# Optimization experiments

Measured on AMD Instinct MI355X. Metric: run time of the kernel, lower is better.

## Reference

```python
import jax, jax.numpy as jnp
import numpy as np

GROUP_SIZE = 64

def setup_inputs() -> dict:
    key = jax.random.key(0)
    ks = jax.random.split(key, 7)
    T, N, K, NG = 4096, 4096, 11264, 4096 // GROUP_SIZE
    x = jax.random.normal(ks[0], (T, N), dtype=jnp.float32)
    Q = jax.random.randint(ks[1], (K, N), 0, 8, dtype=jnp.int32)  # uint8 3-bit codes
    scales = jax.random.uniform(ks[2], (K, NG), dtype=jnp.float32)
    zeros = jax.random.uniform(ks[3], (K, NG), dtype=jnp.float32) * 7.0
    mu1 = jax.random.uniform(ks[4], (N,), dtype=jnp.float32) + 0.5
    mu2 = jax.random.uniform(ks[5], (K,), dtype=jnp.float32) + 0.5
    bias = jax.random.normal(ks[6], (K,), dtype=jnp.float32)
    return {"x": x, "Q": Q, "scales": scales, "zeros": zeros, "mu1": mu1, "mu2": mu2, "bias": bias}

def reference(x, Q, scales, zeros, mu1, mu2, bias):
    K, N = Q.shape
    ng = scales.shape[1]
    # group-wise dequant: (Q - zero) * scale, groups along N
    Qg = Q.astype(jnp.float32).reshape(K, ng, GROUP_SIZE)
    W_deq_norm = ((Qg - zeros[:, :, None]) * scales[:, :, None]).reshape(K, N)
    # Sinkhorn mu rescale: per-row mu2, per-column mu1
    W_deq = W_deq_norm * mu2[:, None] * mu1[None, :]
    out = x @ W_deq.T + bias
    return out
```

## Files before the change

kernel.cpp:

```cpp
#include <hip/hip_runtime.h>
#include <stdint.h>
#include <stddef.h>


typedef __attribute__((ext_vector_type(8))) short bfrag;
typedef __attribute__((ext_vector_type(4))) short s16x4;
typedef __attribute__((ext_vector_type(4))) float f32x4;
typedef __attribute__((ext_vector_type(4))) int   i32x4;

__device__ __forceinline__ short f2bf(float f) {
    uint32_t u = __float_as_uint(f);
    u += 0x7fffu + ((u >> 16) & 1u);
    return (short)(u >> 16);
}

__device__ __forceinline__ void gload_lds16(const void* g, void* l) {
    __builtin_amdgcn_global_load_lds(
        (const __attribute__((address_space(1))) void*)g,
        (__attribute__((address_space(3))) void*)l,
        16, 0, 0);
}

__global__ void cvt_x_kernel(const float* __restrict__ x, short* __restrict__ xb,
                             int total4) {
    for (int i = blockIdx.x * 256 + threadIdx.x; i < total4;
         i += gridDim.x * 256) {
        f32x4 a = ((const f32x4*)x)[i];
        s16x4 o;
        o[0] = f2bf(a[0]); o[1] = f2bf(a[1]);
        o[2] = f2bf(a[2]); o[3] = f2bf(a[3]);
        ((s16x4*)xb)[i] = o;
    }
}

__global__ void deq_w_kernel(const int* __restrict__ Q,
                             const float* __restrict__ scales,
                             const float* __restrict__ zeros,
                             const float* __restrict__ mu1,
                             const float* __restrict__ mu2,
                             short* __restrict__ wb,
                             int k0, int N, int NG) {
    const int kl = blockIdx.x;
    const int kg = k0 + kl;
    const float m2 = mu2[kg];
    const int*   qrow = Q + (size_t)kg * N;
    const float* srow = scales + (size_t)kg * NG;
    const float* zrow = zeros + (size_t)kg * NG;
    short*       orow = wb + (size_t)kl * N;
    for (int n0 = threadIdx.x * 4; n0 < N; n0 += 1024) {
        const int g = n0 >> 6;
        const float s = srow[g] * m2;
        const float z = zrow[g];
        i32x4 q = *(const i32x4*)(qrow + n0);
        f32x4 u = *(const f32x4*)(mu1 + n0);
        s16x4 o;
        o[0] = f2bf(((float)q[0] - z) * s * u[0]);
        o[1] = f2bf(((float)q[1] - z) * s * u[1]);
        o[2] = f2bf(((float)q[2] - z) * s * u[2]);
        o[3] = f2bf(((float)q[3] - z) * s * u[3]);
        *(s16x4*)(orow + n0) = o;
    }
}


__global__ __launch_bounds__(512, 2)
void gemm8p_kernel(const short* __restrict__ A, const short* __restrict__ B,
                   const float* __restrict__ bias, float* __restrict__ C,
                   int Kc, int Nout, int col0, int GX) {
    extern __shared__ __attribute__((aligned(16))) char smem[];

    const int tid  = threadIdx.x;
    const int lane = tid & 63;
    const int wid  = tid >> 6;
    const int wm   = wid >> 2;
    const int wn   = wid & 3;
    const int r    = lane & 15;
    const int hib  = (lane >> 4) << 4;
    const int sw   = (r & 7) << 4;

    const int nwg = (int)gridDim.x;
    const int cpx = nwg >> 3;
    const int bid = (int)blockIdx.x;
    const int swz = (bid & 7) * cpx + (bid >> 3);
    const int bx  = swz % GX;
    const int by  = swz / GX;
    const int bm  = by * 256;
    const int bnl = bx * 256;

    const int KB = Kc * 2;
    const int swcol = ((tid ^ (tid >> 3)) & 7) << 4;
    const char* srcA = (const char*)A + (size_t)(bm  + (tid >> 3)) * KB + swcol;
    const char* srcB = (const char*)B + (size_t)(bnl + (tid >> 3)) * KB + swcol;

    f32x4 acc[8][4];
#pragma unroll
    for (int i = 0; i < 8; i++)
#pragma unroll
        for (int j = 0; j < 4; j++)
            acc[i][j] = (f32x4){0.f, 0.f, 0.f, 0.f};

    const int NT = Kc / 64;

#define STG_A(t, q) gload_lds16(srcA + (size_t)(t) * 128 + (size_t)(q) * 64 * KB, \
                                smem + ((t) & 1) * 65536 + (q) * 8192 + (tid << 4))
#define STG_B(t, q) gload_lds16(srcB + (size_t)(t) * 128 + (size_t)(q) * 64 * KB, \
                                smem + ((t) & 1) * 65536 + 32768 + (q) * 8192 + (tid << 4))
#define LDF(base, row, s) (*(const bfrag*)((base) + (size_t)(row) * 128 + (((s) * 64 + hib) ^ sw)))
#define MM(I, J, AF, BF) acc[I][J] = __builtin_amdgcn_mfma_f32_16x16x32_bf16(AF, BF, acc[I][J], 0, 0, 0)

#define RD_A(Ab_, MQ) do { const int ra_ = wm * 128 + (MQ) * 64 + r;            \
    Af[0] = LDF(Ab_, ra_,      0); Af[1] = LDF(Ab_, ra_,      1);               \
    Af[2] = LDF(Ab_, ra_ + 16, 0); Af[3] = LDF(Ab_, ra_ + 16, 1);               \
    Af[4] = LDF(Ab_, ra_ + 32, 0); Af[5] = LDF(Ab_, ra_ + 32, 1);               \
    Af[6] = LDF(Ab_, ra_ + 48, 0); Af[7] = LDF(Ab_, ra_ + 48, 1); } while (0)

#define RD_B(Bb_, NQ, BF) do { const int rb_ = wn * 64 + (NQ) * 32 + r;         \
    BF[0] = LDF(Bb_, rb_,      0); BF[1] = LDF(Bb_, rb_,      1);               \
    BF[2] = LDF(Bb_, rb_ + 16, 0); BF[3] = LDF(Bb_, rb_ + 16, 1); } while (0)

#define QUAD(MQ, NQ, BF) do {                                                   \
    __builtin_amdgcn_s_barrier();                                               \
    asm volatile("s_waitcnt lgkmcnt(0)" ::: "memory");                          \
    __builtin_amdgcn_s_setprio(1);                                              \
    MM((MQ)*4 + 0, (NQ)*2 + 0, Af[0], BF[0]); MM((MQ)*4 + 0, (NQ)*2 + 0, Af[1], BF[1]); \
    MM((MQ)*4 + 0, (NQ)*2 + 1, Af[0], BF[2]); MM((MQ)*4 + 0, (NQ)*2 + 1, Af[1], BF[3]); \
    MM((MQ)*4 + 1, (NQ)*2 + 0, Af[2], BF[0]); MM((MQ)*4 + 1, (NQ)*2 + 0, Af[3], BF[1]); \
    MM((MQ)*4 + 1, (NQ)*2 + 1, Af[2], BF[2]); MM((MQ)*4 + 1, (NQ)*2 + 1, Af[3], BF[3]); \
    MM((MQ)*4 + 2, (NQ)*2 + 0, Af[4], BF[0]); MM((MQ)*4 + 2, (NQ)*2 + 0, Af[5], BF[1]); \
    MM((MQ)*4 + 2, (NQ)*2 + 1, Af[4], BF[2]); MM((MQ)*4 + 2, (NQ)*2 + 1, Af[5], BF[3]); \
    MM((MQ)*4 + 3, (NQ)*2 + 0, Af[6], BF[0]); MM((MQ)*4 + 3, (NQ)*2 + 0, Af[7], BF[1]); \
    MM((MQ)*4 + 3, (NQ)*2 + 1, Af[6], BF[2]); MM((MQ)*4 + 3, (NQ)*2 + 1, Af[7], BF[3]); \
    __builtin_amdgcn_s_setprio(0);                                              \
} while (0)

    STG_A(0, 0); STG_A(0, 1); STG_A(0, 2); STG_A(0, 3);
    STG_B(0, 0); STG_B(0, 1); STG_B(0, 2); STG_B(0, 3);
    STG_A(1, 0); STG_A(1, 2);
    asm volatile("s_waitcnt vmcnt(2)" ::: "memory");
    __builtin_amdgcn_s_barrier();

    bfrag Af[8], B0f[4], B1f[4];

    for (int it = 0; it < NT / 2; ++it) {
        const int tb = 2 * it + 1;
        int tc = 2 * it + 2; if (tc > NT - 1) tc = NT - 1;
        int td = 2 * it + 3; if (td > NT - 1) td = NT - 1;
        const char* Ab0 = smem;
        const char* Bb0 = smem + 32768;
        const char* Ab1 = smem + 65536;
        const char* Bb1 = smem + 98304;

        RD_A(Ab0, 0); RD_B(Bb0, 0, B0f);
        STG_A(tb, 1); STG_A(tb, 3); STG_B(tb, 0);
        QUAD(0, 0, B0f);
        __builtin_amdgcn_s_barrier();

        RD_B(Bb0, 1, B1f);
        STG_B(tb, 1); STG_B(tb, 2); STG_B(tb, 3);
        QUAD(0, 1, B1f);
        __builtin_amdgcn_s_barrier();

        RD_A(Ab0, 1);
        STG_A(tc, 0); STG_A(tc, 2);
        QUAD(1, 1, B1f);
        __builtin_amdgcn_s_barrier();

        QUAD(1, 0, B0f);
        asm volatile("s_waitcnt vmcnt(2)" ::: "memory");
        __builtin_amdgcn_s_barrier();

        RD_A(Ab1, 0); RD_B(Bb1, 0, B0f);
        STG_A(tc, 1); STG_A(tc, 3); STG_B(tc, 0);
        QUAD(0, 0, B0f);
        __builtin_amdgcn_s_barrier();

        RD_B(Bb1, 1, B1f);
        STG_B(tc, 1); STG_B(tc, 2); STG_B(tc, 3);
        QUAD(0, 1, B1f);
        __builtin_amdgcn_s_barrier();

        RD_A(Ab1, 1);
        STG_A(td, 0); STG_A(td, 2);
        QUAD(1, 1, B1f);
        __builtin_amdgcn_s_barrier();

        QUAD(1, 0, B0f);
        asm volatile("s_waitcnt vmcnt(2)" ::: "memory");
        __builtin_amdgcn_s_barrier();
    }

#undef QUAD
#undef RD_B
#undef RD_A
#undef MM
#undef LDF
#undef STG_B
#undef STG_A

    const int row0 = bm + wm * 128 + (lane >> 4) * 4;
    const int colg = col0 + bnl + wn * 64 + r;
#pragma unroll
    for (int j = 0; j < 4; ++j) {
        const int col = colg + j * 16;
        const float bv = bias[col];
#pragma unroll
        for (int i = 0; i < 8; ++i) {
            const int row = row0 + i * 16;
#pragma unroll
            for (int q = 0; q < 4; ++q)
                C[(size_t)(row + q) * Nout + col] = acc[i][j][q] + bv;
        }
    }
}

__global__ void naive_kernel(const float* __restrict__ x, const int* __restrict__ Q,
                             const float* __restrict__ scales, const float* __restrict__ zeros,
                             const float* __restrict__ mu1, const float* __restrict__ mu2,
                             const float* __restrict__ bias, float* __restrict__ out,
                             int T, int N, int K, int NG) {
    long long total = (long long)T * K;
    for (long long idx = blockIdx.x * 256ll + threadIdx.x; idx < total;
         idx += (long long)gridDim.x * 256ll) {
        int t = (int)(idx / K);
        int k = (int)(idx - (long long)t * K);
        float s = 0.f;
        for (int n = 0; n < N; n++) {
            int g = n >> 6;
            float w = ((float)Q[(size_t)k * N + n] - zeros[(size_t)k * NG + g]) *
                      scales[(size_t)k * NG + g];
            s += x[(size_t)t * N + n] * w * mu1[n];
        }
        out[idx] = s * mu2[k] + bias[k];
    }
}

extern "C" void kernel_launch(void* const* d_in, const int* in_sizes, int n_in,
                              void* d_out, int out_size, void* d_ws, size_t ws_size,
                              hipStream_t stream) {
    const float* x      = (const float*)d_in[0];
    const int*   Q      = (const int*)d_in[1];
    const float* scales = (const float*)d_in[2];
    const float* zeros  = (const float*)d_in[3];
    const float* mu1    = (const float*)d_in[4];
    const float* mu2    = (const float*)d_in[5];
    const float* bias   = (const float*)d_in[6];
    float* out = (float*)d_out;

    const int N  = in_sizes[4];
    const int K  = in_sizes[5];
    const int T  = in_sizes[0] / N;
    const int NG = in_sizes[2] / K;

    const size_t xb_bytes  = (size_t)T * N * 2;
    const size_t row_bytes = (size_t)N * 2;

    const bool shape_ok = (T % 256 == 0) && (K % 256 == 0) &&
                          (N % 1024 == 0) && (N % 128 == 0);

    if (!shape_ok || ws_size < xb_bytes + 256 * row_bytes) {
        naive_kernel<<<4096, 256, 0, stream>>>(x, Q, scales, zeros, mu1, mu2,
                                               bias, out, T, N, K, NG);
        return;
    }

    static bool attr_done = false;
    if (!attr_done) {
        (void)hipFuncSetAttribute(reinterpret_cast<const void*>(gemm8p_kernel),
                                  hipFuncAttributeMaxDynamicSharedMemorySize,
                                  131072);
        attr_done = true;
    }

    short* xb = (short*)d_ws;
    short* wb = (short*)((char*)d_ws + xb_bytes);
    size_t max_rows = (ws_size - xb_bytes) / row_bytes;
    int CH = (int)((max_rows / 256) * 256);
    if (CH > K) CH = K;

    cvt_x_kernel<<<2048, 256, 0, stream>>>(x, xb, T * (N / 4));

    for (int c0 = 0; c0 < K; c0 += CH) {
        int rows = (K - c0 < CH) ? (K - c0) : CH;
        deq_w_kernel<<<rows, 256, 0, stream>>>(Q, scales, zeros, mu1, mu2, wb,
                                               c0, N, NG);
        const int GX = rows / 256;
        dim3 ggrid(GX * (T / 256));
        gemm8p_kernel<<<ggrid, 512, 131072, stream>>>(xb, wb, bias, out,
                                                      N, K, c0, GX);
    }
}
```

Baseline: 684.9 us.

## Switch GEMM to 32x32x16 MFMA and restructure dequant grid over columns

The GEMM inner loop moves from 16x16x32 bf16 MFMA to 32x32x16 bf16 MFMA, with fragment reads, accumulator layout, the quad schedule (two quads per tile instead of four) and the epilogue row mapping rewritten to match. The aim is fewer MFMA issues and fewer LDS fragment reads per tile, with the larger instruction giving more reuse per operand. The dequant kernel now uses a 2D grid where each thread keeps its mu1 slice and loops over a band of rows, reducing redundant mu1 loads. Risks include register pressure from 16-wide accumulators and new LDS bank patterns from the changed swizzle, and the dequant assumes rows divisible by 128.

Result: slower. 754.3 us (+10.1%).

```diff
diff --git a/kernel.cpp b/kernel.cpp
--- a/kernel.cpp
+++ b/kernel.cpp
@@ -3,10 +3,11 @@
 #include <stddef.h>
 
 
-typedef __attribute__((ext_vector_type(8))) short bfrag;
-typedef __attribute__((ext_vector_type(4))) short s16x4;
-typedef __attribute__((ext_vector_type(4))) float f32x4;
-typedef __attribute__((ext_vector_type(4))) int   i32x4;
+typedef __attribute__((ext_vector_type(8)))  short bfrag;
+typedef __attribute__((ext_vector_type(4)))  short s16x4;
+typedef __attribute__((ext_vector_type(4)))  float f32x4;
+typedef __attribute__((ext_vector_type(16))) float f32x16;
+typedef __attribute__((ext_vector_type(4)))  int   i32x4;
 
 __device__ __forceinline__ short f2bf(float f) {
     uint32_t u = __float_as_uint(f);
@@ -39,26 +40,23 @@
                              const float* __restrict__ mu1,
                              const float* __restrict__ mu2,
                              short* __restrict__ wb,
-                             int k0, int N, int NG) {
-    const int kl = blockIdx.x;
-    const int kg = k0 + kl;
-    const float m2 = mu2[kg];
-    const int*   qrow = Q + (size_t)kg * N;
-    const float* srow = scales + (size_t)kg * NG;
-    const float* zrow = zeros + (size_t)kg * NG;
-    short*       orow = wb + (size_t)kl * N;
-    for (int n0 = threadIdx.x * 4; n0 < N; n0 += 1024) {
-        const int g = n0 >> 6;
-        const float s = srow[g] * m2;
-        const float z = zrow[g];
-        i32x4 q = *(const i32x4*)(qrow + n0);
-        f32x4 u = *(const f32x4*)(mu1 + n0);
+                             int k0, int rows, int N, int NG) {
+    const int n0 = blockIdx.x * 1024 + threadIdx.x * 4;
+    const int g  = n0 >> 6;
+    const int KR = rows >> 7;
+    const int kb = blockIdx.y * KR;
+    const f32x4 u = *(const f32x4*)(mu1 + n0);
+    for (int k = kb; k < kb + KR; ++k) {
+        const int kg = k0 + k;
+        const float s = scales[(size_t)kg * NG + g] * mu2[kg];
+        const float z = zeros[(size_t)kg * NG + g];
+        i32x4 q = *(const i32x4*)(Q + (size_t)kg * N + n0);
         s16x4 o;
         o[0] = f2bf(((float)q[0] - z) * s * u[0]);
         o[1] = f2bf(((float)q[1] - z) * s * u[1]);
         o[2] = f2bf(((float)q[2] - z) * s * u[2]);
         o[3] = f2bf(((float)q[3] - z) * s * u[3]);
-        *(s16x4*)(orow + n0) = o;
+        *(s16x4*)(wb + (size_t)k * N + n0) = o;
     }
 }
 
@@ -69,14 +67,14 @@
                    int Kc, int Nout, int col0, int GX) {
     extern __shared__ __attribute__((aligned(16))) char smem[];
 
-    const int tid  = threadIdx.x;
-    const int lane = tid & 63;
-    const int wid  = tid >> 6;
-    const int wm   = wid >> 2;
-    const int wn   = wid & 3;
-    const int r    = lane & 15;
-    const int hib  = (lane >> 4) << 4;
-    const int sw   = (r & 7) << 4;
+    const int tid   = threadIdx.x;
+    const int lane  = tid & 63;
+    const int wid   = tid >> 6;
+    const int wm    = wid >> 2;
+    const int wn    = wid & 3;
+    const int l31   = lane & 31;
+    const int hib   = (lane >> 5) << 4;
+    const int sw    = (lane & 7) << 4;
 
     const int nwg = (int)gridDim.x;
     const int cpx = nwg >> 3;
@@ -92,12 +90,14 @@
     const char* srcA = (const char*)A + (size_t)(bm  + (tid >> 3)) * KB + swcol;
     const char* srcB = (const char*)B + (size_t)(bnl + (tid >> 3)) * KB + swcol;
 
-    f32x4 acc[8][4];
-#pragma unroll
-    for (int i = 0; i < 8; i++)
-#pragma unroll
-        for (int j = 0; j < 4; j++)
-            acc[i][j] = (f32x4){0.f, 0.f, 0.f, 0.f};
+    f32x16 acc[4][2];
+#pragma unroll
+    for (int i = 0; i < 4; i++)
+#pragma unroll
+        for (int j = 0; j < 2; j++)
+#pragma unroll
+            for (int e = 0; e < 16; e++)
+                acc[i][j][e] = 0.f;
 
     const int NT = Kc / 64;
 
@@ -105,31 +105,33 @@
                                 smem + ((t) & 1) * 65536 + (q) * 8192 + (tid << 4))
 #define STG_B(t, q) gload_lds16(srcB + (size_t)(t) * 128 + (size_t)(q) * 64 * KB, \
                                 smem + ((t) & 1) * 65536 + 32768 + (q) * 8192 + (tid << 4))
-#define LDF(base, row, s) (*(const bfrag*)((base) + (size_t)(row) * 128 + (((s) * 64 + hib) ^ sw)))
-#define MM(I, J, AF, BF) acc[I][J] = __builtin_amdgcn_mfma_f32_16x16x32_bf16(AF, BF, acc[I][J], 0, 0, 0)
-
-#define RD_A(Ab_, MQ) do { const int ra_ = wm * 128 + (MQ) * 64 + r;            \
+#define LDF(base, row, ks) (*(const bfrag*)((base) + (size_t)(row) * 128 + ((((ks) << 5) + hib) ^ sw)))
+#define MM(I, J, AF, BF) acc[I][J] = __builtin_amdgcn_mfma_f32_32x32x16_bf16(AF, BF, acc[I][J], 0, 0, 0)
+
+#define RD_A(Ab_, MQ) do { const int ra_ = wm * 128 + (MQ) * 64 + l31;          \
     Af[0] = LDF(Ab_, ra_,      0); Af[1] = LDF(Ab_, ra_,      1);               \
-    Af[2] = LDF(Ab_, ra_ + 16, 0); Af[3] = LDF(Ab_, ra_ + 16, 1);               \
+    Af[2] = LDF(Ab_, ra_,      2); Af[3] = LDF(Ab_, ra_,      3);               \
     Af[4] = LDF(Ab_, ra_ + 32, 0); Af[5] = LDF(Ab_, ra_ + 32, 1);               \
-    Af[6] = LDF(Ab_, ra_ + 48, 0); Af[7] = LDF(Ab_, ra_ + 48, 1); } while (0)
-
-#define RD_B(Bb_, NQ, BF) do { const int rb_ = wn * 64 + (NQ) * 32 + r;         \
-    BF[0] = LDF(Bb_, rb_,      0); BF[1] = LDF(Bb_, rb_,      1);               \
-    BF[2] = LDF(Bb_, rb_ + 16, 0); BF[3] = LDF(Bb_, rb_ + 16, 1); } while (0)
-
-#define QUAD(MQ, NQ, BF) do {                                                   \
+    Af[6] = LDF(Ab_, ra_ + 32, 2); Af[7] = LDF(Ab_, ra_ + 32, 3); } while (0)
+
+#define RD_B(Bb_) do { const int rb_ = wn * 64 + l31;                           \
+    Bf[0] = LDF(Bb_, rb_,      0); Bf[1] = LDF(Bb_, rb_,      1);               \
+    Bf[2] = LDF(Bb_, rb_,      2); Bf[3] = LDF(Bb_, rb_,      3);               \
+    Bf[4] = LDF(Bb_, rb_ + 32, 0); Bf[5] = LDF(Bb_, rb_ + 32, 1);               \
+    Bf[6] = LDF(Bb_, rb_ + 32, 2); Bf[7] = LDF(Bb_, rb_ + 32, 3); } while (0)
+
+#define QUAD(MQ) do {                                                           \
     __builtin_amdgcn_s_barrier();                                               \
     asm volatile("s_waitcnt lgkmcnt(0)" ::: "memory");                          \
     __builtin_amdgcn_s_setprio(1);                                              \
-    MM((MQ)*4 + 0, (NQ)*2 + 0, Af[0], BF[0]); MM((MQ)*4 + 0, (NQ)*2 + 0, Af[1], BF[1]); \
-    MM((MQ)*4 + 0, (NQ)*2 + 1, Af[0], BF[2]); MM((MQ)*4 + 0, (NQ)*2 + 1, Af[1], BF[3]); \
-    MM((MQ)*4 + 1, (NQ)*2 + 0, Af[2], BF[0]); MM((MQ)*4 + 1, (NQ)*2 + 0, Af[3], BF[1]); \
-    MM((MQ)*4 + 1, (NQ)*2 + 1, Af[2], BF[2]); MM((MQ)*4 + 1, (NQ)*2 + 1, Af[3], BF[3]); \
-    MM((MQ)*4 + 2, (NQ)*2 + 0, Af[4], BF[0]); MM((MQ)*4 + 2, (NQ)*2 + 0, Af[5], BF[1]); \
-    MM((MQ)*4 + 2, (NQ)*2 + 1, Af[4], BF[2]); MM((MQ)*4 + 2, (NQ)*2 + 1, Af[5], BF[3]); \
-    MM((MQ)*4 + 3, (NQ)*2 + 0, Af[6], BF[0]); MM((MQ)*4 + 3, (NQ)*2 + 0, Af[7], BF[1]); \
-    MM((MQ)*4 + 3, (NQ)*2 + 1, Af[6], BF[2]); MM((MQ)*4 + 3, (NQ)*2 + 1, Af[7], BF[3]); \
+    MM((MQ)*2 + 0, 0, Af[0], Bf[0]); MM((MQ)*2 + 0, 1, Af[0], Bf[4]);           \
+    MM((MQ)*2 + 1, 0, Af[4], Bf[0]); MM((MQ)*2 + 1, 1, Af[4], Bf[4]);           \
+    MM((MQ)*2 + 0, 0, Af[1], Bf[1]); MM((MQ)*2 + 0, 1, Af[1], Bf[5]);           \
+    MM((MQ)*2 + 1, 0, Af[5], Bf[1]); MM((MQ)*2 + 1, 1, Af[5], Bf[5]);           \
+    MM((MQ)*2 + 0, 0, Af[2], Bf[2]); MM((MQ)*2 + 0, 1, Af[2], Bf[6]);           \
+    MM((MQ)*2 + 1, 0, Af[6], Bf[2]); MM((MQ)*2 + 1, 1, Af[6], Bf[6]);           \
+    MM((MQ)*2 + 0, 0, Af[3], Bf[3]); MM((MQ)*2 + 0, 1, Af[3], Bf[7]);           \
+    MM((MQ)*2 + 1, 0, Af[7], Bf[3]); MM((MQ)*2 + 1, 1, Af[7], Bf[7]);           \
     __builtin_amdgcn_s_setprio(0);                                              \
 } while (0)
 
@@ -139,7 +141,7 @@
     asm volatile("s_waitcnt vmcnt(2)" ::: "memory");
     __builtin_amdgcn_s_barrier();
 
-    bfrag Af[8], B0f[4], B1f[4];
+    bfrag Af[8], Bf[8];
 
     for (int it = 0; it < NT / 2; ++it) {
         const int tb = 2 * it + 1;
@@ -150,41 +152,25 @@
         const char* Ab1 = smem + 65536;
         const char* Bb1 = smem + 98304;
 
-        RD_A(Ab0, 0); RD_B(Bb0, 0, B0f);
-        STG_A(tb, 1); STG_A(tb, 3); STG_B(tb, 0);
-        QUAD(0, 0, B0f);
-        __builtin_amdgcn_s_barrier();
-
-        RD_B(Bb0, 1, B1f);
-        STG_B(tb, 1); STG_B(tb, 2); STG_B(tb, 3);
-        QUAD(0, 1, B1f);
+        RD_A(Ab0, 0); RD_B(Bb0);
+        STG_A(tb, 1); STG_A(tb, 3); STG_B(tb, 0); STG_B(tb, 1);
+        QUAD(0);
         __builtin_amdgcn_s_barrier();
 
         RD_A(Ab0, 1);
-        STG_A(tc, 0); STG_A(tc, 2);
-        QUAD(1, 1, B1f);
-        __builtin_amdgcn_s_barrier();
-
-        QUAD(1, 0, B0f);
+        STG_B(tb, 2); STG_B(tb, 3); STG_A(tc, 0); STG_A(tc, 2);
+        QUAD(1);
         asm volatile("s_waitcnt vmcnt(2)" ::: "memory");
         __builtin_amdgcn_s_barrier();
 
-        RD_A(Ab1, 0); RD_B(Bb1, 0, B0f);
-        STG_A(tc, 1); STG_A(tc, 3); STG_B(tc, 0);
-        QUAD(0, 0, B0f);
-        __builtin_amdgcn_s_barrier();
-
-        RD_B(Bb1, 1, B1f);
-        STG_B(tc, 1); STG_B(tc, 2); STG_B(tc, 3);
-        QUAD(0, 1, B1f);
+        RD_A(Ab1, 0); RD_B(Bb1);
+        STG_A(tc, 1); STG_A(tc, 3); STG_B(tc, 0); STG_B(tc, 1);
+        QUAD(0);
         __builtin_amdgcn_s_barrier();
 
         RD_A(Ab1, 1);
-        STG_A(td, 0); STG_A(td, 2);
-        QUAD(1, 1, B1f);
-        __builtin_amdgcn_s_barrier();
-
-        QUAD(1, 0, B0f);
+        STG_B(tc, 2); STG_B(tc, 3); STG_A(td, 0); STG_A(td, 2);
+        QUAD(1);
         asm volatile("s_waitcnt vmcnt(2)" ::: "memory");
         __builtin_amdgcn_s_barrier();
     }
@@ -197,18 +183,19 @@
 #undef STG_B
 #undef STG_A
 
-    const int row0 = bm + wm * 128 + (lane >> 4) * 4;
-    const int colg = col0 + bnl + wn * 64 + r;
-#pragma unroll
-    for (int j = 0; j < 4; ++j) {
-        const int col = colg + j * 16;
+    const int rql = 4 * (lane >> 5);
+#pragma unroll
+    for (int j = 0; j < 2; ++j) {
+        const int col = col0 + bnl + wn * 64 + j * 32 + l31;
         const float bv = bias[col];
 #pragma unroll
-        for (int i = 0; i < 8; ++i) {
-            const int row = row0 + i * 16;
-#pragma unroll
-            for (int q = 0; q < 4; ++q)
-                C[(size_t)(row + q) * Nout + col] = acc[i][j][q] + bv;
+        for (int i = 0; i < 4; ++i) {
+            const int rowb = bm + wm * 128 + i * 32 + rql;
+#pragma unroll
+            for (int reg = 0; reg < 16; ++reg) {
+                const int row = rowb + (reg & 3) + 8 * (reg >> 2);
+                C[(size_t)row * Nout + col] = acc[i][j][reg] + bv;
+            }
         }
     }
 }
@@ -281,8 +268,9 @@
 
     for (int c0 = 0; c0 < K; c0 += CH) {
         int rows = (K - c0 < CH) ? (K - c0) : CH;
-        deq_w_kernel<<<rows, 256, 0, stream>>>(Q, scales, zeros, mu1, mu2, wb,
-                                               c0, N, NG);
+        dim3 dgrid(N / 1024, 128);
+        deq_w_kernel<<<dgrid, 256, 0, stream>>>(Q, scales, zeros, mu1, mu2, wb,
+                                                c0, rows, N, NG);
         const int GX = rows / 256;
         dim3 ggrid(GX * (T / 256));
         gemm8p_kernel<<<ggrid, 512, 131072, stream>>>(xb, wb, bias, out,
```
